# Performance work log

Hardware: AMD Instinct MI355X
Metric: run time of the kernel (lower is better)

The kernel has to match this reference:

```python
import jax, jax.numpy as jnp
import numpy as np

C, N, H = 1024, 64, 16
B, T = 4, 1024
DECAY_LORA, AAA_LORA, MV_LORA, GATE_LORA = 64, 64, 32, 128
EPS_GN = 0.00064


def setup_inputs() -> dict:
    key = jax.random.key(0)
    ks = iter(jax.random.split(key, 32))
    nrm = lambda shape, s=0.02: jax.random.normal(next(ks), shape, jnp.float32) * s
    uni = lambda shape: jax.random.uniform(next(ks), shape, jnp.float32)
    inp = {
        'x': jax.random.normal(next(ks), (B, T, C), jnp.float32),
        'x_r': uni((1, 1, C)), 'x_w': uni((1, 1, C)), 'x_k': uni((1, 1, C)),
        'x_v': uni((1, 1, C)), 'x_a': uni((1, 1, C)), 'x_g': uni((1, 1, C)),
        'w0': nrm((1, 1, C), 0.5), 'w1': nrm((C, DECAY_LORA)), 'w2': nrm((DECAY_LORA, C)),
        'a0': nrm((1, 1, C), 0.5), 'a1': nrm((C, AAA_LORA)), 'a2': nrm((AAA_LORA, C)),
        'v0': nrm((1, 1, C), 0.5), 'v1': nrm((C, MV_LORA)), 'v2': nrm((MV_LORA, C)),
        'g1': nrm((C, GATE_LORA)), 'g2': nrm((GATE_LORA, C)),
        'k_k': uni((1, 1, C)), 'k_a': uni((1, 1, C)), 'r_k': nrm((H, N), 0.1),
        'Wr': nrm((C, C)), 'Wk': nrm((C, C)), 'Wv': nrm((C, C)), 'Wo': nrm((C, C)),
        'ln_gamma': jnp.ones((C,), jnp.float32), 'ln_beta': jnp.zeros((C,), jnp.float32),
    }
    return inp


def rwkv7_op(r, w, k, v, a, b):
    # r,w,k,v,a,b: [B,T,C]; state S: [B,H,N,N] (rows=value dim, cols=key dim)
    Bb, Tt, Cc = r.shape
    to_t = lambda z: z.reshape(Bb, Tt, H, N).transpose(1, 0, 2, 3)  # [T,B,H,N]
    r_, k_, v_, a_, b_ = map(to_t, (r, k, v, a, b))
    w_ = jnp.exp(-jnp.exp(to_t(w)))  # decay in (0,1)
    def step(S, inp):
        rt, wt, kt, vt, at, bt = inp
        sa = jnp.einsum('bhij,bhj->bhi', S, at)                 # S @ a
        S = S * wt[:, :, None, :] + sa[..., None] * bt[:, :, None, :] \
            + vt[..., None] * kt[:, :, None, :]
        out = jnp.einsum('bhij,bhj->bhi', S, rt)
        return S, out
    S0 = jnp.zeros((Bb, H, N, N), r.dtype)
    _, outs = jax.lax.scan(step, S0, (r_, w_, k_, v_, a_, b_))
    return outs.transpose(1, 0, 2, 3).reshape(Bb, Tt, Cc)


def reference(x, x_r, x_w, x_k, x_v, x_a, x_g, w0, w1, w2, a0, a1, a2,
              v0, v1, v2, g1, g2, k_k, k_a, r_k, Wr, Wk, Wv, Wo,
              ln_gamma, ln_beta):
    Bb, Tt, Cc = x.shape
    # token shift
    xx = jnp.pad(x, ((0, 0), (1, 0), (0, 0)))[:, :-1] - x
    xr = x + xx * x_r; xw = x + xx * x_w; xk = x + xx * x_k
    xv = x + xx * x_v; xa = x + xx * x_a; xg = x + xx * x_g
    r = xr @ Wr
    w = -jax.nn.softplus(-(w0 + jnp.tanh(xw @ w1) @ w2)) - 0.5
    k = xk @ Wk
    v = xv @ Wv
    v_first = v  # first-layer case (v_first=None)
    a = jax.nn.sigmoid(a0 + xa @ a1 @ a2)
    g = jax.nn.sigmoid(xg @ g1) @ g2
    kk = k * k_k
    kkh = kk.reshape(Bb, Tt, H, N)
    kk = (kkh / jnp.maximum(jnp.linalg.norm(kkh, axis=-1, keepdims=True), 1e-12)).reshape(Bb, Tt, Cc)
    k = k * (1 + (a - 1) * k_a)
    o = rwkv7_op(r, w, k, v, -kk, kk * a)
    # group norm over H groups of N channels
    y = o.reshape(Bb * Tt, H, N)
    mu = jnp.mean(y, axis=-1, keepdims=True)
    var = jnp.var(y, axis=-1, keepdims=True)
    y = ((y - mu) * jax.lax.rsqrt(var + EPS_GN)).reshape(Bb, Tt, Cc) * ln_gamma + ln_beta
    rh = r.reshape(Bb, Tt, H, N)
    kh = k.reshape(Bb, Tt, H, N)
    vh = v.reshape(Bb, Tt, H, N)
    rwkv = jnp.sum(rh * kh * r_k, axis=-1, keepdims=True) * vh
    y = y + rwkv.reshape(Bb, Tt, Cc)
    out = (y * g) @ Wo
    return out, v_first
```

## Files before the change

### kernel.cpp

```cpp
#include <hip/hip_runtime.h>
#include <hip/hip_bf16.h>
#include <math.h>

#define BB 4
#define TT 1024
#define CCH 1024
#define HH 16
#define NNd 64
#define PAD 65
#define RS 72
#define LBS 68

typedef short bf16x8 __attribute__((ext_vector_type(8)));
typedef float f32x4 __attribute__((ext_vector_type(4)));

__device__ __forceinline__ unsigned short f2bf(float f) {
  __hip_bfloat16 h = __float2bfloat16(f);
  return __builtin_bit_cast(unsigned short, h);
}
__device__ __forceinline__ float bf2f(unsigned short u) {
  unsigned int x = (unsigned int)u << 16;
  return __builtin_bit_cast(float, x);
}
__device__ __forceinline__ float sigmoidf_(float x) {
  return __builtin_amdgcn_rcpf(1.0f + __expf(-x));
}
__device__ __forceinline__ float ftanh_(float x) {
  return 1.0f - 2.0f * __builtin_amdgcn_rcpf(__expf(2.0f * x) + 1.0f);
}

__device__ __forceinline__ void gl2lds16(const unsigned short* g, unsigned short* l) {
  __builtin_amdgcn_global_load_lds(
      (const __attribute__((address_space(1))) unsigned int*)g,
      (__attribute__((address_space(3))) unsigned int*)l, 16, 0, 0);
}

__device__ __forceinline__ void transpose_tile(
    const float* __restrict__ in, unsigned short* __restrict__ out,
    int R, int Cc, int r0, int c0, unsigned short (*tile)[68], int t)
{
  const int rr = t >> 4;
  const int cc = (t & 15) * 4;
#pragma unroll
  for (int p = 0; p < 4; ++p) {
    int row = p * 16 + rr;
    float4 v = *(const float4*)(in + (size_t)(r0 + row) * Cc + c0 + cc);
    tile[row][cc]     = f2bf(v.x);
    tile[row][cc + 1] = f2bf(v.y);
    tile[row][cc + 2] = f2bf(v.z);
    tile[row][cc + 3] = f2bf(v.w);
  }
  __syncthreads();
#pragma unroll
  for (int p = 0; p < 4; ++p) {
    int row = p * 16 + rr;
    ushort4 o;
    o.x = tile[cc][row];
    o.y = tile[cc + 1][row];
    o.z = tile[cc + 2][row];
    o.w = tile[cc + 3][row];
    *(ushort4*)(out + (size_t)(c0 + row) * R + r0 + cc) = o;
  }
}

__global__ __launch_bounds__(256) void prep_kernel(
    const float* __restrict__ x,
    const float* __restrict__ cr, const float* __restrict__ cw,
    const float* __restrict__ ck, const float* __restrict__ cv,
    const float* __restrict__ ca, const float* __restrict__ cg,
    unsigned short* __restrict__ xr, unsigned short* __restrict__ xw,
    unsigned short* __restrict__ xk, unsigned short* __restrict__ xv,
    unsigned short* __restrict__ xa, unsigned short* __restrict__ xg,
    const float* __restrict__ W0, const float* __restrict__ W1,
    const float* __restrict__ W2, const float* __restrict__ W3,
    unsigned short* __restrict__ T0, unsigned short* __restrict__ T1,
    unsigned short* __restrict__ T2, unsigned short* __restrict__ T3,
    const float* __restrict__ w1, const float* __restrict__ w2,
    const float* __restrict__ a1, const float* __restrict__ a2,
    const float* __restrict__ g1, const float* __restrict__ g2,
    unsigned short* __restrict__ w1T, unsigned short* __restrict__ w2T,
    unsigned short* __restrict__ a1T, unsigned short* __restrict__ a2T,
    unsigned short* __restrict__ g1T, unsigned short* __restrict__ g2T)
{
  __shared__ unsigned short tile[64][68];
  const int blk = blockIdx.x;
  const int tid = threadIdx.x;
  if (blk < 4096) {
    const size_t idx = ((size_t)blk * 256 + tid) * 4;
    const int c = (int)(idx & 1023);
    const int t = (int)((idx >> 10) & 1023);
    float4 xc = *(const float4*)(x + idx);
    float4 xp = make_float4(0.f, 0.f, 0.f, 0.f);
    if (t > 0) xp = *(const float4*)(x + idx - 1024);
    float4 dx = make_float4(xp.x - xc.x, xp.y - xc.y, xp.z - xc.z, xp.w - xc.w);
    auto st = [&](unsigned short* dst, const float* coef) {
      float4 w = *(const float4*)(coef + c);
      ushort4 o;
      o.x = f2bf(fmaf(dx.x, w.x, xc.x));
      o.y = f2bf(fmaf(dx.y, w.y, xc.y));
      o.z = f2bf(fmaf(dx.z, w.z, xc.z));
      o.w = f2bf(fmaf(dx.w, w.w, xc.w));
      *(ushort4*)(dst + idx) = o;
    };
    st(xr, cr); st(xw, cw); st(xk, ck); st(xv, cv); st(xa, ca); st(xg, cg);
  } else if (blk < 5120) {
    const int j = blk - 4096;
    const int z = j >> 8, rem = j & 255;
    const int ty = rem >> 4, tx = rem & 15;
    const float* src = (z == 0) ? W0 : (z == 1) ? W1 : (z == 2) ? W2 : W3;
    unsigned short* dst = (z == 0) ? T0 : (z == 1) ? T1 : (z == 2) ? T2 : T3;
    transpose_tile(src, dst, 1024, 1024, tx * 64, ty * 64, tile, tid);
  } else {
    const int i = blk - 5120;
    const float* src; unsigned short* dst; int R, C, rt, ct;
    if (i < 16)      { src = w1; dst = w1T; R = 1024; C = 64;   rt = i;      ct = 0; }
    else if (i < 32) { src = w2; dst = w2T; R = 64;   C = 1024; rt = 0;      ct = i - 16; }
    else if (i < 48) { src = a1; dst = a1T; R = 1024; C = 64;   rt = i - 32; ct = 0; }
    else if (i < 64) { src = a2; dst = a2T; R = 64;   C = 1024; rt = 0;      ct = i - 48; }
    else if (i < 96) { int k = i - 64; src = g1; dst = g1T; R = 1024; C = 128; rt = k >> 1; ct = k & 1; }
    else             { int k = i - 96; src = g2; dst = g2T; R = 128; C = 1024; rt = k & 1;  ct = k >> 1; }
    transpose_tile(src, dst, R, C, rt * 64, ct * 64, tile, tid);
  }
}

__global__ __launch_bounds__(256) void gemm_stage1_kernel(
    const unsigned short* __restrict__ xrB, const unsigned short* __restrict__ xkB,
    const unsigned short* __restrict__ xvB,
    const unsigned short* __restrict__ WrT, const unsigned short* __restrict__ WkT,
    const unsigned short* __restrict__ WvT,
    unsigned short* __restrict__ r_btc, unsigned short* __restrict__ k_btc,
    float* __restrict__ v_btc,
    const unsigned short* __restrict__ xwB, const unsigned short* __restrict__ xaB,
    const unsigned short* __restrict__ xgB,
    const unsigned short* __restrict__ w1T, const unsigned short* __restrict__ a1T,
    const unsigned short* __restrict__ g1T,
    unsigned short* __restrict__ hwB, unsigned short* __restrict__ haB,
    unsigned short* __restrict__ hgB)
{
  constexpr int K = 1024, SK = 32;
  __shared__ __align__(16) unsigned short As[128 * SK];
  __shared__ __align__(16) unsigned short Bs[128 * SK];
  const int blk = blockIdx.x;
  const int tid = threadIdx.x;
  const int wv = tid >> 6, lane = tid & 63;
  const int fr = lane & 15, q = lane >> 4;
  const int arow = tid >> 2;
  const int akc = (tid & 3) * 8;

  if (blk < 768) {
    const int z = blk >> 8, rem = blk & 255;
    const int m0 = (rem & 31) * 128;
    const int n0 = (rem >> 5) * 128;
    const unsigned short* A = (z == 0) ? xrB : (z == 1) ? xkB : xvB;
    const unsigned short* BT = (z == 0) ? WrT : (z == 1) ? WkT : WvT;
    const int wave_m = wv >> 1, wave_n = wv & 1;

    f32x4 acc[4][4];
#pragma unroll
    for (int i = 0; i < 4; i++)
#pragma unroll
      for (int j = 0; j < 4; j++) acc[i][j] = (f32x4){0.f, 0.f, 0.f, 0.f};

    for (int k0 = 0; k0 < K; k0 += 32) {
#pragma unroll
      for (int i = 0; i < 2; ++i)
        gl2lds16(A + (size_t)(m0 + arow + i * 64) * K + k0 + akc, As + i * 2048 + wv * 512);
#pragma unroll
      for (int i = 0; i < 2; ++i)
        gl2lds16(BT + (size_t)(n0 + arow + i * 64) * K + k0 + akc, Bs + i * 2048 + wv * 512);
      __syncthreads();
      bf16x8 af[4], bfv[4];
#pragma unroll
      for (int i = 0; i < 4; i++)
        af[i] = *(const bf16x8*)(&As[(wave_m * 64 + i * 16 + fr) * SK + q * 8]);
#pragma unroll
      for (int j = 0; j < 4; j++)
        bfv[j] = *(const bf16x8*)(&Bs[(wave_n * 64 + j * 16 + fr) * SK + q * 8]);
#pragma unroll
      for (int i = 0; i < 4; i++)
#pragma unroll
        for (int j = 0; j < 4; j++)
          acc[i][j] = __builtin_amdgcn_mfma_f32_16x16x32_bf16(af[i], bfv[j], acc[i][j], 0, 0, 0);
      __syncthreads();
    }
#pragma unroll
    for (int i = 0; i < 4; i++)
#pragma unroll
      for (int j = 0; j < 4; j++) {
        const int mb = m0 + wave_m * 64 + i * 16 + q * 4;
        const int n = n0 + wave_n * 64 + j * 16 + fr;
#pragma unroll
        for (int r = 0; r < 4; r++) {
          if (z == 0)      r_btc[(size_t)(mb + r) * 1024 + n] = f2bf(acc[i][j][r]);
          else if (z == 1) k_btc[(size_t)(mb + r) * 1024 + n] = f2bf(acc[i][j][r]);
          else             v_btc[(size_t)(mb + r) * 1024 + n] = acc[i][j][r];
        }
      }
  } else {
    const int j2 = blk - 768;
    const int y = j2 >> 5;
    const int m0 = (j2 & 31) * 128;
    const unsigned short* A  = (y == 0) ? xwB : (y == 1) ? xaB : xgB;
    const unsigned short* BT = (y == 0) ? w1T : (y == 1) ? a1T : (g1T + (size_t)(y - 2) * 64 * K);
    unsigned short* outb = (y == 0) ? hwB : (y == 1) ? haB : hgB;
    const int Nout = (y < 2) ? 64 : 128;
    const int ncol0 = (y < 2) ? 0 : (y - 2) * 64;

    f32x4 acc[2][4];
#pragma unroll
    for (int i = 0; i < 2; i++)
#pragma unroll
      for (int j = 0; j < 4; j++) acc[i][j] = (f32x4){0.f, 0.f, 0.f, 0.f};

    for (int k0 = 0; k0 < K; k0 += 32) {
#pragma unroll
      for (int i = 0; i < 2; ++i)
        gl2lds16(A + (size_t)(m0 + arow + i * 64) * K + k0 + akc, As + i * 2048 + wv * 512);
      gl2lds16(BT + (size_t)arow * K + k0 + akc, Bs + wv * 512);
      __syncthreads();
      bf16x8 af[2], bfv[4];
#pragma unroll
      for (int i = 0; i < 2; i++)
        af[i] = *(const bf16x8*)(&As[(wv * 32 + i * 16 + fr) * SK + q * 8]);
#pragma unroll
      for (int j = 0; j < 4; j++)
        bfv[j] = *(const bf16x8*)(&Bs[(j * 16 + fr) * SK + q * 8]);
#pragma unroll
      for (int i = 0; i < 2; i++)
#pragma unroll
        for (int j = 0; j < 4; j++)
          acc[i][j] = __builtin_amdgcn_mfma_f32_16x16x32_bf16(af[i], bfv[j], acc[i][j], 0, 0, 0);
      __syncthreads();
    }
#pragma unroll
    for (int i = 0; i < 2; i++)
#pragma unroll
      for (int j = 0; j < 4; j++) {
        const int mb = m0 + wv * 32 + i * 16 + q * 4;
        const int n = ncol0 + j * 16 + fr;
#pragma unroll
        for (int r = 0; r < 4; r++) {
          float val = acc[i][j][r];
          if (y == 0) val = ftanh_(val);
          else if (y >= 2) val = sigmoidf_(val);
          outb[(size_t)(mb + r) * Nout + n] = f2bf(val);
        }
      }
  }
}

__global__ __launch_bounds__(256) void lora2_kernel(
    const unsigned short* __restrict__ hwB, const unsigned short* __restrict__ haB,
    const unsigned short* __restrict__ hgB,
    const unsigned short* __restrict__ w2T, const unsigned short* __restrict__ a2T,
    const unsigned short* __restrict__ g2T,
    unsigned short* __restrict__ wraw, unsigned short* __restrict__ araw,
    unsigned short* __restrict__ gfB)
{
  constexpr int N = 1024, SK = 32;
  __shared__ __align__(16) unsigned short As[128 * SK];
  __shared__ __align__(16) unsigned short Bs[128 * SK];
  const int z = blockIdx.z;
  const unsigned short* A = (z == 0) ? hwB : (z == 1) ? haB : hgB;
  const unsigned short* BT = (z == 0) ? w2T : (z == 1) ? a2T : g2T;
  unsigned short* out = (z == 0) ? wraw : (z == 1) ? araw : gfB;
  const int K = (z == 2) ? 128 : 64;

  const int tid = threadIdx.x;
  const int wv = tid >> 6, lane = tid & 63;
  const int fr = lane & 15, q = lane >> 4;
  const int wave_m = wv >> 1, wave_n = wv & 1;
  const int m0 = blockIdx.x * 128;
  const int n0 = blockIdx.y * 128;

  f32x4 acc[4][4];
#pragma unroll
  for (int i = 0; i < 4; i++)
#pragma unroll
    for (int j = 0; j < 4; j++) acc[i][j] = (f32x4){0.f, 0.f, 0.f, 0.f};

  const int arow = tid >> 2;
  const int akc = (tid & 3) * 8;

  for (int k0 = 0; k0 < K; k0 += 32) {
#pragma unroll
    for (int i = 0; i < 2; ++i)
      gl2lds16(A + (size_t)(m0 + arow + i * 64) * K + k0 + akc, As + i * 2048 + wv * 512);
#pragma unroll
    for (int i = 0; i < 2; ++i)
      gl2lds16(BT + (size_t)(n0 + arow + i * 64) * K + k0 + akc, Bs + i * 2048 + wv * 512);
    __syncthreads();
    bf16x8 af[4], bfv[4];
#pragma unroll
    for (int i = 0; i < 4; i++)
      af[i] = *(const bf16x8*)(&As[(wave_m * 64 + i * 16 + fr) * SK + q * 8]);
#pragma unroll
    for (int j = 0; j < 4; j++)
      bfv[j] = *(const bf16x8*)(&Bs[(wave_n * 64 + j * 16 + fr) * SK + q * 8]);
#pragma unroll
    for (int i = 0; i < 4; i++)
#pragma unroll
      for (int j = 0; j < 4; j++)
        acc[i][j] = __builtin_amdgcn_mfma_f32_16x16x32_bf16(af[i], bfv[j], acc[i][j], 0, 0, 0);
    __syncthreads();
  }
#pragma unroll
  for (int i = 0; i < 4; i++)
#pragma unroll
    for (int j = 0; j < 4; j++) {
      const int mb = m0 + wave_m * 64 + i * 16 + q * 4;
      const int n = n0 + wave_n * 64 + j * 16 + fr;
#pragma unroll
      for (int r = 0; r < 4; r++)
        out[(size_t)(mb + r) * N + n] = f2bf(acc[i][j][r]);
    }
}

__global__ __launch_bounds__(256) void gemm_out_kernel(
    const unsigned short* __restrict__ A,
    const unsigned short* __restrict__ BT,
    float* __restrict__ out)
{
  constexpr int K = 1024, N = 1024, SK = 32;
  __shared__ __align__(16) unsigned short As[128 * SK];
  __shared__ __align__(16) unsigned short Bs[128 * SK];
  const int tid = threadIdx.x;
  const int wv = tid >> 6, lane = tid & 63;
  const int fr = lane & 15, q = lane >> 4;
  const int wave_m = wv >> 1, wave_n = wv & 1;
  const int m0 = blockIdx.x * 128;
  const int n0 = blockIdx.y * 128;

  f32x4 acc[4][4];
#pragma unroll
  for (int i = 0; i < 4; i++)
#pragma unroll
    for (int j = 0; j < 4; j++) acc[i][j] = (f32x4){0.f, 0.f, 0.f, 0.f};

  const int arow = tid >> 2;
  const int akc = (tid & 3) * 8;

  for (int k0 = 0; k0 < K; k0 += 32) {
#pragma unroll
    for (int i = 0; i < 2; ++i)
      gl2lds16(A + (size_t)(m0 + arow + i * 64) * K + k0 + akc, As + i * 2048 + wv * 512);
#pragma unroll
    for (int i = 0; i < 2; ++i)
      gl2lds16(BT + (size_t)(n0 + arow + i * 64) * K + k0 + akc, Bs + i * 2048 + wv * 512);
    __syncthreads();
    bf16x8 af[4], bfv[4];
#pragma unroll
    for (int i = 0; i < 4; i++)
      af[i] = *(const bf16x8*)(&As[(wave_m * 64 + i * 16 + fr) * SK + q * 8]);
#pragma unroll
    for (int j = 0; j < 4; j++)
      bfv[j] = *(const bf16x8*)(&Bs[(wave_n * 64 + j * 16 + fr) * SK + q * 8]);
#pragma unroll
    for (int i = 0; i < 4; i++)
#pragma unroll
      for (int j = 0; j < 4; j++)
        acc[i][j] = __builtin_amdgcn_mfma_f32_16x16x32_bf16(af[i], bfv[j], acc[i][j], 0, 0, 0);
    __syncthreads();
  }
#pragma unroll
  for (int i = 0; i < 4; i++)
#pragma unroll
    for (int j = 0; j < 4; j++) {
      const int mb = m0 + wave_m * 64 + i * 16 + q * 4;
      const int n = n0 + wave_n * 64 + j * 16 + fr;
#pragma unroll
      for (int r = 0; r < 4; r++)
        out[(size_t)(mb + r) * N + n] = acc[i][j][r];
    }
}

__global__ __launch_bounds__(256, 2) void chunk_ops_kernel(
    const unsigned short* __restrict__ r_btc, const unsigned short* __restrict__ k_btc,
    const float* __restrict__ v_btc, const unsigned short* __restrict__ wraw,
    const unsigned short* __restrict__ araw,
    const float* __restrict__ w0, const float* __restrict__ a0,
    const float* __restrict__ k_k, const float* __restrict__ k_a,
    const float* __restrict__ r_k,
    unsigned short* __restrict__ McG, unsigned short* __restrict__ NcG,
    unsigned short* __restrict__ PcG, unsigned short* __restrict__ OlG,
    unsigned short* __restrict__ DkG, float* __restrict__ s3G)
{
  extern __shared__ char smraw[];
  unsigned short* AHb  = (unsigned short*)smraw;
  unsigned short* RHb  = AHb + 64 * RS;
  unsigned short* BPb  = RHb + 64 * RS;
  unsigned short* KPb  = BPb + 64 * RS;
  unsigned short* BPTb = KPb + 64 * RS;
  unsigned short* KPTb = BPTb + 64 * RS;
  unsigned short* VSTb = KPTb + 64 * RS;
  unsigned short* LBb  = VSTb + 64 * RS;
  float* GLs = (float*)(LBb + 64 * LBS);
  float* SS  = GLs + 64;
  unsigned short* XTb = AHb;
  unsigned short* LKb = BPb;
  unsigned short* QTb = BPb;
  unsigned short* DBb = KPb;

  const int inst = blockIdx.x;
  const int bh = inst >> 4, c = inst & 15;
  const int b = bh >> 4, h = bh & 15;
  const int tid = threadIdx.x;
  const int lane = tid & 63;
  const int wv = tid >> 6;
  const int jl = lane;
  const int ch = h * 64 + jl;
  const size_t base = ((size_t)(b * 1024 + c * 64) * 1024) + ch;

  const float p_w0 = w0[ch], p_a0 = a0[ch];
  const float p_kk = k_k[ch], p_ka = k_a[ch], p_rk = r_k[ch];
  const float EM = 0.60653065971263342f;

  unsigned short wr_u[16], kv_u[16], rv_u[16], ar_u[16];
  float vv_u[16];
#pragma unroll
  for (int u = 0; u < 16; ++u) {
    const size_t gi = base + (size_t)(16 * wv + u) * 1024;
    wr_u[u] = wraw[gi];
    kv_u[u] = k_btc[gi];
    rv_u[u] = r_btc[gi];
    ar_u[u] = araw[gi];
    vv_u[u] = v_btc[gi];
  }

  float lwv[16];
  {
    float run = 0.f;
#pragma unroll
    for (int u = 0; u < 16; ++u) {
      run += -EM * sigmoidf_(p_w0 + bf2f(wr_u[u]));
      lwv[u] = run;
    }
    SS[wv * 64 + jl] = run;
  }
  __syncthreads();
  const float s0 = SS[0 * 64 + jl], s1 = SS[1 * 64 + jl];
  const float s2 = SS[2 * 64 + jl], s3s = SS[3 * 64 + jl];
  const float goff = (wv > 0 ? s0 : 0.f) + (wv > 1 ? s1 : 0.f) + (wv > 2 ? s2 : 0.f);
  const float gl = s0 + s1 + s2 + s3s;
  if (wv == 0) GLs[jl] = gl;

  float s3v[16];
  {
    const float e_gl = __expf(gl);
#pragma unroll
    for (int u = 0; u < 16; ++u) {
      const int t = 16 * wv + u;
      const float pre = goff + (u ? lwv[u - 1] : 0.f);
      const float cur = goff + lwv[u];
      const float kv = bf2f(kv_u[u]), rv = bf2f(rv_u[u]);
      const float vv = vv_u[u];
      const float av = sigmoidf_(p_a0 + bf2f(ar_u[u]));
      const float kkx = kv * p_kk;
      float ssq = kkx * kkx;
#pragma unroll
      for (int m = 1; m < 64; m <<= 1) ssq += __shfl_xor(ssq, m);
      const float scale = __builtin_amdgcn_rsqf(fmaxf(ssq, 1e-24f));
      const float kkn = kkx * scale;
      const float bb = kkn * av;
      const float kmod = kv * (1.0f + (av - 1.0f) * p_ka);
      float s3 = rv * kmod * p_rk;
#pragma unroll
      for (int m = 1; m < 64; m <<= 1) s3 += __shfl_xor(s3, m);
      s3v[u] = s3;
      const float e_prev = __expf(pre);
      const float e_gu   = __expf(cur);
      const float em     = __expf(-cur);
      const float egl    = e_gl * em;
      AHb[t * RS + jl] = f2bf(-kkn * e_prev);
      BPb[t * RS + jl] = f2bf(bb * em);
      KPb[t * RS + jl] = f2bf(kmod * em);
      BPTb[jl * RS + t] = f2bf(bb * egl);
      KPTb[jl * RS + t] = f2bf(kmod * egl);
      RHb[t * RS + jl] = f2bf(rv * e_gu);
      VSTb[jl * RS + t] = f2bf(vv);
    }
    if (jl == 0) {
      float* sp = s3G + (bh << 10) + (c << 6) + 16 * wv;
#pragma unroll
      for (int k2 = 0; k2 < 4; ++k2)
        *(float4*)(sp + 4 * k2) = make_float4(s3v[4 * k2], s3v[4 * k2 + 1],
                                              s3v[4 * k2 + 2], s3v[4 * k2 + 3]);
    }
  }
  __syncthreads();

  const int fr = lane & 15, q = lane >> 4;
  const int i0 = wv * 16;

  {
    f32x4 aLB[4], aLK[4], aDB[4], aDK[4];
#pragma unroll
    for (int j = 0; j < 4; ++j) {
      aLB[j] = (f32x4){0.f, 0.f, 0.f, 0.f}; aLK[j] = (f32x4){0.f, 0.f, 0.f, 0.f};
      aDB[j] = (f32x4){0.f, 0.f, 0.f, 0.f}; aDK[j] = (f32x4){0.f, 0.f, 0.f, 0.f};
    }
#pragma unroll
    for (int ks = 0; ks < 2; ++ks) {
      const int ko = ks * 32 + q * 8;
      bf16x8 fA = *(const bf16x8*)(AHb + (i0 + fr) * RS + ko);
      bf16x8 fR = *(const bf16x8*)(RHb + (i0 + fr) * RS + ko);
#pragma unroll
      for (int j = 0; j < 4; ++j) {
        bf16x8 fB = *(const bf16x8*)(BPb + (j * 16 + fr) * RS + ko);
        bf16x8 fK = *(const bf16x8*)(KPb + (j * 16 + fr) * RS + ko);
        aLB[j] = __builtin_amdgcn_mfma_f32_16x16x32_bf16(fA, fB, aLB[j], 0, 0, 0);
        aLK[j] = __builtin_amdgcn_mfma_f32_16x16x32_bf16(fA, fK, aLK[j], 0, 0, 0);
        aDB[j] = __builtin_amdgcn_mfma_f32_16x16x32_bf16(fR, fB, aDB[j], 0, 0, 0);
        aDK[j] = __builtin_amdgcn_mfma_f32_16x16x32_bf16(fR, fK, aDK[j], 0, 0, 0);
      }
    }
    __syncthreads();
#pragma unroll
    for (int j = 0; j < 4; ++j) {
      const int s = j * 16 + fr;
#pragma unroll
      for (int r = 0; r < 4; ++r) {
        const int t = i0 + q * 4 + r;
        LBb[t * LBS + s] = f2bf((s < t) ? aLB[j][r] : 0.f);
        LKb[t * RS + s] = f2bf((s < t) ? aLK[j][r] : 0.f);
        DBb[t * RS + s] = f2bf((s <= t) ? aDB[j][r] : 0.f);
        DkG[(size_t)inst * 4096 + t * 64 + s] = f2bf((s <= t) ? aDK[j][r] : 0.f);
      }
    }
  }
  __syncthreads();

  {
    f32x4 wacc[4];
#pragma unroll
    for (int j = 0; j < 4; ++j) wacc[j] = (f32x4){0.f, 0.f, 0.f, 0.f};
#pragma unroll
    for (int ks = 0; ks < 2; ++ks) {
      const int ko = ks * 32 + q * 8;
      bf16x8 fL = *(const bf16x8*)(LKb + (i0 + fr) * RS + ko);
#pragma unroll
      for (int j = 0; j < 4; ++j) {
        bf16x8 fV = *(const bf16x8*)(VSTb + (j * 16 + fr) * RS + ko);
        wacc[j] = __builtin_amdgcn_mfma_f32_16x16x32_bf16(fL, fV, wacc[j], 0, 0, 0);
      }
    }
#pragma unroll
    for (int j = 0; j < 4; ++j)
#pragma unroll
      for (int r = 0; r < 4; ++r)
        LKb[(i0 + q * 4 + r) * RS + j * 16 + fr] = f2bf(wacc[j][r]);
  }
  __syncthreads();

  bf16x8 fDK0, fDK1;
  {
    const unsigned short* dkp = DkG + (size_t)inst * 4096 + (i0 + fr) * 64 + q * 8;
    fDK0 = *(const bf16x8*)(dkp);
    fDK1 = *(const bf16x8*)(dkp + 32);
  }

  if (wv < 2) {
    const int jc = lane;
    unsigned short* Sb = (wv == 0) ? AHb : LKb;
    unsigned short* Tb = (wv == 0) ? XTb : QTb;
    float x[64];
#pragma unroll
    for (int t = 0; t < 64; ++t) x[t] = bf2f(Sb[t * RS + jc]);
#pragma unroll
    for (int z2 = 0; z2 < 8; ++z2)
      *(bf16x8*)(Tb + jc * RS + z2 * 8) = (bf16x8){0, 0, 0, 0, 0, 0, 0, 0};

    const int jf = jc & 15, tjm = jc >> 4;

#pragma unroll
    for (int I = 0; I < 4; ++I) {
      if (I > 0) {
        f32x4 cU[4];
#pragma unroll
        for (int tj = 0; tj < 4; ++tj) cU[tj] = (f32x4){0.f, 0.f, 0.f, 0.f};
#pragma unroll
        for (int kw = 0; kw < 2; ++kw) {
          if (kw * 32 < 16 * I) {
            const int ko = kw * 32 + q * 8;
            bf16x8 fL;
            *(ushort4*)&fL = *(const ushort4*)(LBb + (16 * I + fr) * LBS + ko);
            *((ushort4*)&fL + 1) = *(const ushort4*)(LBb + (16 * I + fr) * LBS + ko + 4);
#pragma unroll
            for (int tj = 0; tj < 4; ++tj) {
              bf16x8 fX = *(const bf16x8*)(Tb + (tj * 16 + fr) * RS + ko);
              cU[tj] = __builtin_amdgcn_mfma_f32_16x16x32_bf16(fL, fX, cU[tj], 0, 0, 0);
            }
          }
        }
#pragma unroll
        for (int qq = 0; qq < 4; ++qq) {
          const int saddr = (qq * 16 + jf) * 4;
#pragma unroll
          for (int r = 0; r < 4; ++r) {
            int g0 = __builtin_amdgcn_ds_bpermute(saddr, __builtin_bit_cast(int, cU[0][r]));
            int g1 = __builtin_amdgcn_ds_bpermute(saddr, __builtin_bit_cast(int, cU[1][r]));
            int g2 = __builtin_amdgcn_ds_bpermute(saddr, __builtin_bit_cast(int, cU[2][r]));
            int g3 = __builtin_amdgcn_ds_bpermute(saddr, __builtin_bit_cast(int, cU[3][r]));
            int gs = (tjm == 0) ? g0 : (tjm == 1) ? g1 : (tjm == 2) ? g2 : g3;
            x[16 * I + qq * 4 + r] += __builtin_bit_cast(float, gs);
          }
        }
      }
#pragma unroll
      for (int u = 1; u < 16; ++u) {
        const unsigned short* lr = LBb + (16 * I + u) * LBS + 16 * I;
        float acc0 = 0.f, acc1 = 0.f;
#pragma unroll
        for (int s = 0; s + 2 <= u; s += 2) {
          acc0 = fmaf(bf2f(lr[s]), x[16 * I + s], acc0);
          acc1 = fmaf(bf2f(lr[s + 1]), x[16 * I + s + 1], acc1);
        }
        if (u & 1) acc0 = fmaf(bf2f(lr[u - 1]), x[16 * I + u - 1], acc0);
        x[16 * I + u] += acc0 + acc1;
      }
#pragma unroll
      for (int t2 = 0; t2 < 16; t2 += 2) {
        unsigned int pk = (unsigned int)f2bf(x[16 * I + t2])
                        | ((unsigned int)f2bf(x[16 * I + t2 + 1]) << 16);
        *(unsigned int*)(Tb + jc * RS + 16 * I + t2) = pk;
      }
    }
  }
  __syncthreads();

  {
    f32x4 mA[4], nA[4], pA[4], oA[4];
#pragma unroll
    for (int j = 0; j < 4; ++j) {
      mA[j] = (f32x4){0.f, 0.f, 0.f, 0.f}; nA[j] = (f32x4){0.f, 0.f, 0.f, 0.f};
      pA[j] = (f32x4){0.f, 0.f, 0.f, 0.f}; oA[j] = (f32x4){0.f, 0.f, 0.f, 0.f};
    }
#pragma unroll
    for (int ks = 0; ks < 2; ++ks) {
      const int ko = ks * 32 + q * 8;
      bf16x8 fBT = *(const bf16x8*)(BPTb + (i0 + fr) * RS + ko);
      bf16x8 fKT = *(const bf16x8*)(KPTb + (i0 + fr) * RS + ko);
      bf16x8 fDB = *(const bf16x8*)(DBb + (i0 + fr) * RS + ko);
      bf16x8 fDK = ks ? fDK1 : fDK0;
#pragma unroll
      for (int j = 0; j < 4; ++j) {
        bf16x8 fXT = *(const bf16x8*)(XTb + (j * 16 + fr) * RS + ko);
        bf16x8 fQT = *(const bf16x8*)(QTb + (j * 16 + fr) * RS + ko);
        bf16x8 fVT = *(const bf16x8*)(VSTb + (j * 16 + fr) * RS + ko);
        mA[j] = __builtin_amdgcn_mfma_f32_16x16x32_bf16(fBT, fXT, mA[j], 0, 0, 0);
        nA[j] = __builtin_amdgcn_mfma_f32_16x16x32_bf16(fBT, fQT, nA[j], 0, 0, 0);
        nA[j] = __builtin_amdgcn_mfma_f32_16x16x32_bf16(fKT, fVT, nA[j], 0, 0, 0);
        pA[j] = __builtin_amdgcn_mfma_f32_16x16x32_bf16(fDB, fXT, pA[j], 0, 0, 0);
        oA[j] = __builtin_amdgcn_mfma_f32_16x16x32_bf16(fDB, fQT, oA[j], 0, 0, 0);
        oA[j] = __builtin_amdgcn_mfma_f32_16x16x32_bf16(fDK, fVT, oA[j], 0, 0, 0);
      }
    }
    const size_t ob = (size_t)inst * 4096;
    float eg[4];
#pragma unroll
    for (int r = 0; r < 4; ++r) eg[r] = __expf(GLs[i0 + q * 4 + r]);
#pragma unroll
    for (int j = 0; j < 4; ++j) {
      const int col = j * 16 + fr;
#pragma unroll
      for (int r = 0; r < 4; ++r) {
        const int row = i0 + q * 4 + r;
        const size_t oi = ob + (size_t)row * 64 + col;
        McG[oi] = f2bf(mA[j][r] + (row == col ? eg[r] : 0.f));
        NcG[oi] = f2bf(nA[j][r]);
        PcG[oi] = f2bf(pA[j][r] + bf2f(RHb[row * RS + col]));
        OlG[oi] = f2bf(oA[j][r]);
      }
    }
  }
}

__global__ __launch_bounds__(256) void chunk_scan_kernel(
    const unsigned short* __restrict__ McG, const unsigned short* __restrict__ NcG,
    unsigned short* __restrict__ Sch)
{
  __shared__ __align__(16) unsigned short STh[64 * RS];
  __shared__ __align__(16) unsigned short STl[64 * RS];
  const int bh = blockIdx.x;
  const int tid = threadIdx.x;
  const int wv = tid >> 6, lane = tid & 63;
  const int fr = lane & 15, q = lane >> 4;

  f32x4 acc[4];

  {
    const size_t ob = ((size_t)bh << 4) << 12;
#pragma unroll
    for (int j = 0; j < 4; ++j) {
      const int col = j * 16 + fr;
#pragma unroll
      for (int r = 0; r < 4; ++r) {
        const int row = wv * 16 + q * 4 + r;
        Sch[ob + (size_t)row * 64 + col] = 0;
        acc[j][r] = bf2f(NcG[ob + (size_t)row * 64 + col]);
      }
    }
  }

  for (int c = 1; c < 16; ++c) {
    const size_t ob = ((((size_t)bh << 4) + (size_t)c) << 12);
    __syncthreads();
#pragma unroll
    for (int j = 0; j < 4; ++j) {
      const int col = j * 16 + fr;
#pragma unroll
      for (int r = 0; r < 4; ++r) {
        const int row = wv * 16 + q * 4 + r;
        const float v = acc[j][r];
        const unsigned short hi = f2bf(v);
        STh[col * RS + row] = hi;
        STl[col * RS + row] = f2bf(v - bf2f(hi));
        Sch[ob + (size_t)row * 64 + col] = hi;
      }
    }
    __syncthreads();
    const bf16x8 fA0 = *(const bf16x8*)(McG + ob + (size_t)(wv * 16 + fr) * 64 + q * 8);
    const bf16x8 fA1 = *(const bf16x8*)(McG + ob + (size_t)(wv * 16 + fr) * 64 + 32 + q * 8);
#pragma unroll
    for (int j = 0; j < 4; ++j) {
      const int col = j * 16 + fr;
#pragma unroll
      for (int r = 0; r < 4; ++r)
        acc[j][r] = bf2f(NcG[ob + (size_t)(wv * 16 + q * 4 + r) * 64 + col]);
      const bf16x8 h0 = *(const bf16x8*)(STh + (j * 16 + fr) * RS + q * 8);
      const bf16x8 h1 = *(const bf16x8*)(STh + (j * 16 + fr) * RS + 32 + q * 8);
      const bf16x8 l0 = *(const bf16x8*)(STl + (j * 16 + fr) * RS + q * 8);
      const bf16x8 l1 = *(const bf16x8*)(STl + (j * 16 + fr) * RS + 32 + q * 8);
      acc[j] = __builtin_amdgcn_mfma_f32_16x16x32_bf16(fA0, h0, acc[j], 0, 0, 0);
      acc[j] = __builtin_amdgcn_mfma_f32_16x16x32_bf16(fA1, h1, acc[j], 0, 0, 0);
      acc[j] = __builtin_amdgcn_mfma_f32_16x16x32_bf16(fA0, l0, acc[j], 0, 0, 0);
      acc[j] = __builtin_amdgcn_mfma_f32_16x16x32_bf16(fA1, l1, acc[j], 0, 0, 0);
    }
  }
}

__global__ __launch_bounds__(256) void chunk_outgn_kernel(
    const unsigned short* __restrict__ PcG, const unsigned short* __restrict__ OlG,
    const unsigned short* __restrict__ Sch, const float* __restrict__ s3G,
    const float* __restrict__ v_btc, const unsigned short* __restrict__ g_f,
    const float* __restrict__ gamma, const float* __restrict__ beta,
    unsigned short* __restrict__ yg)
{
  __shared__ float ST[64 * PAD];
  __shared__ float PB[64 * PAD];
  const int inst = blockIdx.x;
  const int bh = inst >> 4, c = inst & 15;
  const int b = bh >> 4, h = bh & 15;
  const int tid = threadIdx.x;
  const int tt = tid >> 4, jt = tid & 15;
  const size_t ob = (size_t)inst << 12;

#pragma unroll
  for (int q = 0; q < 4; ++q) {
    int idx = q * 1024 + tid * 4;
    int row = idx >> 6, col = idx & 63;
    ushort4 sv = *(const ushort4*)(Sch + ob + idx);
    ST[row * PAD + col] = bf2f(sv.x);     ST[row * PAD + col + 1] = bf2f(sv.y);
    ST[row * PAD + col + 2] = bf2f(sv.z); ST[row * PAD + col + 3] = bf2f(sv.w);
    ushort4 pv = *(const ushort4*)(PcG + ob + idx);
    PB[row * PAD + col] = bf2f(pv.x);     PB[row * PAD + col + 1] = bf2f(pv.y);
    PB[row * PAD + col + 2] = bf2f(pv.z); PB[row * PAD + col + 3] = bf2f(pv.w);
  }
  __syncthreads();

  float acc[4][4];
#pragma unroll
  for (int u = 0; u < 4; ++u) {
    ushort4 o4 = *(const ushort4*)(OlG + ob + (size_t)(4 * tt + u) * 64 + 4 * jt);
    acc[u][0] = bf2f(o4.x); acc[u][1] = bf2f(o4.y);
    acc[u][2] = bf2f(o4.z); acc[u][3] = bf2f(o4.w);
  }
#pragma unroll 4
  for (int pp = 0; pp < 64; ++pp) {
    float pv[4], sv[4];
#pragma unroll
    for (int u = 0; u < 4; ++u) pv[u] = PB[(4 * tt + u) * PAD + pp];
#pragma unroll
    for (int v = 0; v < 4; ++v) sv[v] = ST[pp * PAD + 4 * jt + v];
#pragma unroll
    for (int u = 0; u < 4; ++u)
#pragma unroll
      for (int v = 0; v < 4; ++v) acc[u][v] = fmaf(pv[u], sv[v], acc[u][v]);
  }

  const int colb = h * 64 + 4 * jt;
  float4 ga4 = *(const float4*)(gamma + colb);
  float4 be4 = *(const float4*)(beta + colb);

#pragma unroll
  for (int u = 0; u < 4; ++u) {
    float sum1 = acc[u][0] + acc[u][1] + acc[u][2] + acc[u][3];
    float sum2 = acc[u][0] * acc[u][0] + acc[u][1] * acc[u][1]
               + acc[u][2] * acc[u][2] + acc[u][3] * acc[u][3];
#pragma unroll
    for (int m = 1; m < 16; m <<= 1) {
      sum1 += __shfl_xor(sum1, m);
      sum2 += __shfl_xor(sum2, m);
    }
    const float mean = sum1 * (1.0f / 64.0f);
    const float var = sum2 * (1.0f / 64.0f) - mean * mean;
    const float rstd = __builtin_amdgcn_rsqf(var + 0.00064f);
    const int tok = c * 64 + 4 * tt + u;
    const float s3 = s3G[(bh << 10) + tok];
    const size_t gaddr = ((size_t)(b * 1024 + tok) * 1024) + colb;
    float4 v4 = *(const float4*)(v_btc + gaddr);
    ushort4 g4b = *(const ushort4*)(g_f + gaddr);
    ushort4 ov;
    ov.x = f2bf(((acc[u][0] - mean) * rstd * ga4.x + be4.x + s3 * v4.x) * bf2f(g4b.x));
    ov.y = f2bf(((acc[u][1] - mean) * rstd * ga4.y + be4.y + s3 * v4.y) * bf2f(g4b.y));
    ov.z = f2bf(((acc[u][2] - mean) * rstd * ga4.z + be4.z + s3 * v4.z) * bf2f(g4b.z));
    ov.w = f2bf(((acc[u][3] - mean) * rstd * ga4.w + be4.w + s3 * v4.w) * bf2f(g4b.w));
    *(ushort4*)(yg + gaddr) = ov;
  }
}

extern "C" void kernel_launch(void* const* d_in, const int* in_sizes, int n_in,
                              void* d_out, int out_size, void* d_ws, size_t ws_size,
                              hipStream_t stream)
{
  (void)in_sizes; (void)n_in; (void)out_size;
  const float* x    = (const float*)d_in[0];
  const float* x_r  = (const float*)d_in[1];
  const float* x_w  = (const float*)d_in[2];
  const float* x_k  = (const float*)d_in[3];
  const float* x_v  = (const float*)d_in[4];
  const float* x_a  = (const float*)d_in[5];
  const float* x_g  = (const float*)d_in[6];
  const float* w0   = (const float*)d_in[7];
  const float* w1   = (const float*)d_in[8];
  const float* w2   = (const float*)d_in[9];
  const float* a0   = (const float*)d_in[10];
  const float* a1   = (const float*)d_in[11];
  const float* a2   = (const float*)d_in[12];
  const float* g1   = (const float*)d_in[16];
  const float* g2   = (const float*)d_in[17];
  const float* k_k  = (const float*)d_in[18];
  const float* k_a  = (const float*)d_in[19];
  const float* r_k  = (const float*)d_in[20];
  const float* Wr   = (const float*)d_in[21];
  const float* Wk   = (const float*)d_in[22];
  const float* Wv   = (const float*)d_in[23];
  const float* Wo   = (const float*)d_in[24];
  const float* ln_g = (const float*)d_in[25];
  const float* ln_b = (const float*)d_in[26];

  float* outp = (float*)d_out;
  float* vfirst = outp + (size_t)BB * TT * CCH;

  char* ws = (char*)d_ws;
  size_t off = 0;
  auto alloc = [&](size_t bytes) -> char* {
    char* p = ws + off;
    off += (bytes + 255) & ~(size_t)255;
    return p;
  };

  unsigned short* WrT = (unsigned short*)alloc(2097152);
  unsigned short* WkT = (unsigned short*)alloc(2097152);
  unsigned short* WvT = (unsigned short*)alloc(2097152);
  unsigned short* WoT = (unsigned short*)alloc(2097152);
  unsigned short* w1T = (unsigned short*)alloc(131072);
  unsigned short* w2T = (unsigned short*)alloc(131072);
  unsigned short* a1T = (unsigned short*)alloc(131072);
  unsigned short* a2T = (unsigned short*)alloc(131072);
  unsigned short* g1T = (unsigned short*)alloc(262144);
  unsigned short* g2T = (unsigned short*)alloc(262144);
  unsigned short* xrB = (unsigned short*)alloc(8388608);
  unsigned short* xwB = (unsigned short*)alloc(8388608);
  unsigned short* xkB = (unsigned short*)alloc(8388608);
  unsigned short* xvB = (unsigned short*)alloc(8388608);
  unsigned short* xaB = (unsigned short*)alloc(8388608);
  unsigned short* xgB = (unsigned short*)alloc(8388608);
  unsigned short* r_btc = (unsigned short*)alloc(8388608);
  unsigned short* k_btc = (unsigned short*)alloc(8388608);
  unsigned short* wraw  = (unsigned short*)alloc(8388608);
  unsigned short* araw  = (unsigned short*)alloc(8388608);
  unsigned short* gfB = (unsigned short*)alloc(8388608);
  unsigned short* OlG = (unsigned short*)alloc(8388608);
  unsigned short* DkG = (unsigned short*)alloc(8388608);
  float* s3G   = (float*)alloc(262144);
  unsigned short* hwB = (unsigned short*)alloc(524288);
  unsigned short* haB = (unsigned short*)alloc(524288);
  unsigned short* hgB = (unsigned short*)alloc(1048576);
  unsigned short* ygB = (unsigned short*)alloc(8388608);

  unsigned short* McG = xrB;
  unsigned short* NcG = xkB;
  unsigned short* PcG = xaB;
  unsigned short* Sch = k_btc;

  if (off > ws_size) return;

  dim3 blk(256);

  prep_kernel<<<5248, blk, 0, stream>>>(
      x, x_r, x_w, x_k, x_v, x_a, x_g,
      xrB, xwB, xkB, xvB, xaB, xgB,
      Wr, Wk, Wv, Wo, WrT, WkT, WvT, WoT,
      w1, w2, a1, a2, g1, g2, w1T, w2T, a1T, a2T, g1T, g2T);

  gemm_stage1_kernel<<<896, blk, 0, stream>>>(
      xrB, xkB, xvB, WrT, WkT, WvT, r_btc, k_btc, vfirst,
      xwB, xaB, xgB, w1T, a1T, g1T, hwB, haB, hgB);

  lora2_kernel<<<dim3(32, 8, 3), blk, 0, stream>>>(
      hwB, haB, hgB, w2T, a2T, g2T, wraw, araw, gfB);

  constexpr int CHUNK_LDS = 7 * 64 * RS * 2 + 64 * LBS * 2 + 64 * 4 + 4 * 64 * 4;
  hipFuncSetAttribute((const void*)chunk_ops_kernel,
                      hipFuncAttributeMaxDynamicSharedMemorySize, CHUNK_LDS);
  chunk_ops_kernel<<<1024, blk, CHUNK_LDS, stream>>>(
      r_btc, k_btc, vfirst, wraw, araw, w0, a0, k_k, k_a, r_k,
      McG, NcG, PcG, OlG, DkG, s3G);

  chunk_scan_kernel<<<64, blk, 0, stream>>>(McG, NcG, Sch);

  chunk_outgn_kernel<<<1024, blk, 0, stream>>>(PcG, OlG, Sch, s3G, vfirst, gfB,
                                               ln_g, ln_b, ygB);

  gemm_out_kernel<<<dim3(32, 8), blk, 0, stream>>>(ygB, WoT, outp);
}
```

Measured before the change: 317.6 us.

## Use MFMA for chunk output GEMM with transposed chunk-state layout

The chunk output kernel now computes P·S with bf16 MFMA instructions straight from global memory, replacing the fp32 shared-memory FMA loop and its staging. To feed the B operand, the scan kernel writes chunk states transposed and packs its shared and global state stores into ushort4 vectors. The epilogue switches to the MFMA fragment layout, which makes the v/g/y global accesses scalar and strided instead of 4-wide vectors. This may cost memory efficiency in the epilogue.

```diff
diff --git a/kernel.cpp b/kernel.cpp
--- a/kernel.cpp
+++ b/kernel.cpp
@@ -7,7 +7,6 @@
 #define CCH 1024
 #define HH 16
 #define NNd 64
-#define PAD 65
 #define RS 72
 #define LBS 68
 
@@ -677,7 +676,7 @@
 
 __global__ __launch_bounds__(256) void chunk_scan_kernel(
     const unsigned short* __restrict__ McG, const unsigned short* __restrict__ NcG,
-    unsigned short* __restrict__ Sch)
+    unsigned short* __restrict__ SchT)
 {
   __shared__ __align__(16) unsigned short STh[64 * RS];
   __shared__ __align__(16) unsigned short STl[64 * RS];
@@ -693,10 +692,11 @@
 #pragma unroll
     for (int j = 0; j < 4; ++j) {
       const int col = j * 16 + fr;
+      *(ushort4*)(SchT + ob + (size_t)col * 64 + wv * 16 + q * 4) =
+          make_ushort4(0, 0, 0, 0);
 #pragma unroll
       for (int r = 0; r < 4; ++r) {
         const int row = wv * 16 + q * 4 + r;
-        Sch[ob + (size_t)row * 64 + col] = 0;
         acc[j][r] = bf2f(NcG[ob + (size_t)row * 64 + col]);
       }
     }
@@ -708,15 +708,20 @@
 #pragma unroll
     for (int j = 0; j < 4; ++j) {
       const int col = j * 16 + fr;
+      ushort4 hs, ls;
 #pragma unroll
       for (int r = 0; r < 4; ++r) {
-        const int row = wv * 16 + q * 4 + r;
         const float v = acc[j][r];
         const unsigned short hi = f2bf(v);
-        STh[col * RS + row] = hi;
-        STl[col * RS + row] = f2bf(v - bf2f(hi));
-        Sch[ob + (size_t)row * 64 + col] = hi;
-      }
+        const unsigned short lo = f2bf(v - bf2f(hi));
+        if (r == 0) { hs.x = hi; ls.x = lo; }
+        else if (r == 1) { hs.y = hi; ls.y = lo; }
+        else if (r == 2) { hs.z = hi; ls.z = lo; }
+        else { hs.w = hi; ls.w = lo; }
+      }
+      *(ushort4*)(STh + col * RS + wv * 16 + q * 4) = hs;
+      *(ushort4*)(STl + col * RS + wv * 16 + q * 4) = ls;
+      *(ushort4*)(SchT + ob + (size_t)col * 64 + wv * 16 + q * 4) = hs;
     }
     __syncthreads();
     const bf16x8 fA0 = *(const bf16x8*)(McG + ob + (size_t)(wv * 16 + fr) * 64 + q * 8);
@@ -741,81 +746,71 @@
 
 __global__ __launch_bounds__(256) void chunk_outgn_kernel(
     const unsigned short* __restrict__ PcG, const unsigned short* __restrict__ OlG,
-    const unsigned short* __restrict__ Sch, const float* __restrict__ s3G,
+    const unsigned short* __restrict__ SchT, const float* __restrict__ s3G,
     const float* __restrict__ v_btc, const unsigned short* __restrict__ g_f,
     const float* __restrict__ gamma, const float* __restrict__ beta,
     unsigned short* __restrict__ yg)
 {
-  __shared__ float ST[64 * PAD];
-  __shared__ float PB[64 * PAD];
   const int inst = blockIdx.x;
   const int bh = inst >> 4, c = inst & 15;
   const int b = bh >> 4, h = bh & 15;
   const int tid = threadIdx.x;
-  const int tt = tid >> 4, jt = tid & 15;
+  const int wv = tid >> 6, lane = tid & 63;
+  const int fr = lane & 15, q = lane >> 4;
+  const int i0 = wv * 16;
   const size_t ob = (size_t)inst << 12;
 
-#pragma unroll
-  for (int q = 0; q < 4; ++q) {
-    int idx = q * 1024 + tid * 4;
-    int row = idx >> 6, col = idx & 63;
-    ushort4 sv = *(const ushort4*)(Sch + ob + idx);
-    ST[row * PAD + col] = bf2f(sv.x);     ST[row * PAD + col + 1] = bf2f(sv.y);
-    ST[row * PAD + col + 2] = bf2f(sv.z); ST[row * PAD + col + 3] = bf2f(sv.w);
-    ushort4 pv = *(const ushort4*)(PcG + ob + idx);
-    PB[row * PAD + col] = bf2f(pv.x);     PB[row * PAD + col + 1] = bf2f(pv.y);
-    PB[row * PAD + col + 2] = bf2f(pv.z); PB[row * PAD + col + 3] = bf2f(pv.w);
-  }
-  __syncthreads();
-
-  float acc[4][4];
-#pragma unroll
-  for (int u = 0; u < 4; ++u) {
-    ushort4 o4 = *(const ushort4*)(OlG + ob + (size_t)(4 * tt + u) * 64 + 4 * jt);
-    acc[u][0] = bf2f(o4.x); acc[u][1] = bf2f(o4.y);
-    acc[u][2] = bf2f(o4.z); acc[u][3] = bf2f(o4.w);
-  }
-#pragma unroll 4
-  for (int pp = 0; pp < 64; ++pp) {
-    float pv[4], sv[4];
-#pragma unroll
-    for (int u = 0; u < 4; ++u) pv[u] = PB[(4 * tt + u) * PAD + pp];
-#pragma unroll
-    for (int v = 0; v < 4; ++v) sv[v] = ST[pp * PAD + 4 * jt + v];
-#pragma unroll
-    for (int u = 0; u < 4; ++u)
-#pragma unroll
-      for (int v = 0; v < 4; ++v) acc[u][v] = fmaf(pv[u], sv[v], acc[u][v]);
-  }
-
-  const int colb = h * 64 + 4 * jt;
-  float4 ga4 = *(const float4*)(gamma + colb);
-  float4 be4 = *(const float4*)(beta + colb);
-
-#pragma unroll
-  for (int u = 0; u < 4; ++u) {
-    float sum1 = acc[u][0] + acc[u][1] + acc[u][2] + acc[u][3];
-    float sum2 = acc[u][0] * acc[u][0] + acc[u][1] * acc[u][1]
-               + acc[u][2] * acc[u][2] + acc[u][3] * acc[u][3];
+  f32x4 acc[4];
+#pragma unroll
+  for (int j = 0; j < 4; ++j) {
+    const int col = j * 16 + fr;
+#pragma unroll
+    for (int r = 0; r < 4; ++r)
+      acc[j][r] = bf2f(OlG[ob + (size_t)(i0 + q * 4 + r) * 64 + col]);
+  }
+  const bf16x8 fA0 = *(const bf16x8*)(PcG + ob + (size_t)(i0 + fr) * 64 + q * 8);
+  const bf16x8 fA1 = *(const bf16x8*)(PcG + ob + (size_t)(i0 + fr) * 64 + 32 + q * 8);
+#pragma unroll
+  for (int j = 0; j < 4; ++j) {
+    const bf16x8 fB0 = *(const bf16x8*)(SchT + ob + (size_t)(j * 16 + fr) * 64 + q * 8);
+    const bf16x8 fB1 = *(const bf16x8*)(SchT + ob + (size_t)(j * 16 + fr) * 64 + 32 + q * 8);
+    acc[j] = __builtin_amdgcn_mfma_f32_16x16x32_bf16(fA0, fB0, acc[j], 0, 0, 0);
+    acc[j] = __builtin_amdgcn_mfma_f32_16x16x32_bf16(fA1, fB1, acc[j], 0, 0, 0);
+  }
+
+  const int colb = h * 64;
+  float ga[4], be[4];
+#pragma unroll
+  for (int j = 0; j < 4; ++j) {
+    ga[j] = gamma[colb + j * 16 + fr];
+    be[j] = beta[colb + j * 16 + fr];
+  }
+
+#pragma unroll
+  for (int r = 0; r < 4; ++r) {
+    float s1 = (acc[0][r] + acc[1][r]) + (acc[2][r] + acc[3][r]);
+    float s2 = (acc[0][r] * acc[0][r] + acc[1][r] * acc[1][r])
+             + (acc[2][r] * acc[2][r] + acc[3][r] * acc[3][r]);
 #pragma unroll
     for (int m = 1; m < 16; m <<= 1) {
-      sum1 += __shfl_xor(sum1, m);
-      sum2 += __shfl_xor(sum2, m);
-    }
-    const float mean = sum1 * (1.0f / 64.0f);
-    const float var = sum2 * (1.0f / 64.0f) - mean * mean;
+      s1 += __shfl_xor(s1, m);
+      s2 += __shfl_xor(s2, m);
+    }
+    const float mean = s1 * (1.0f / 64.0f);
+    const float var = s2 * (1.0f / 64.0f) - mean * mean;
     const float rstd = __builtin_amdgcn_rsqf(var + 0.00064f);
-    const int tok = c * 64 + 4 * tt + u;
+    const int row = i0 + q * 4 + r;
+    const int tok = c * 64 + row;
     const float s3 = s3G[(bh << 10) + tok];
     const size_t gaddr = ((size_t)(b * 1024 + tok) * 1024) + colb;
-    float4 v4 = *(const float4*)(v_btc + gaddr);
-    ushort4 g4b = *(const ushort4*)(g_f + gaddr);
-    ushort4 ov;
-    ov.x = f2bf(((acc[u][0] - mean) * rstd * ga4.x + be4.x + s3 * v4.x) * bf2f(g4b.x));
-    ov.y = f2bf(((acc[u][1] - mean) * rstd * ga4.y + be4.y + s3 * v4.y) * bf2f(g4b.y));
-    ov.z = f2bf(((acc[u][2] - mean) * rstd * ga4.z + be4.z + s3 * v4.z) * bf2f(g4b.z));
-    ov.w = f2bf(((acc[u][3] - mean) * rstd * ga4.w + be4.w + s3 * v4.w) * bf2f(g4b.w));
-    *(ushort4*)(yg + gaddr) = ov;
+#pragma unroll
+    for (int j = 0; j < 4; ++j) {
+      const int col = j * 16 + fr;
+      const float vv = v_btc[gaddr + col];
+      const float gg = bf2f(g_f[gaddr + col]);
+      yg[gaddr + col] =
+          f2bf(((acc[j][r] - mean) * rstd * ga[j] + be[j] + s3 * vv) * gg);
+    }
   }
 }
 
```

Measured after the change: 312.1 us. Within noise of the previous version (-1.7%).
